# Kernel tuning notes

Measured on AMD Instinct MI355X. Metric: run time of the kernel, lower is better.

The kernel has to match this reference:

```python
import jax, jax.numpy as jnp
import numpy as np

D_MODEL = 1024
D_HEAD = 128
B, S = 4, 4096


def apply_rope(x, cos, sin):
    # x: [B,S,d_head], cos/sin: [S, d_head//2]
    half = x.shape[-1] // 2
    x1, x2 = x[..., :half], x[..., half:]
    cos = cos[None, :, :].astype(x.dtype)
    sin = sin[None, :, :].astype(x.dtype)
    return jnp.concatenate([x1 * cos - x2 * sin, x1 * sin + x2 * cos], axis=-1)


def setup_inputs() -> dict:
    key = jax.random.key(0)
    ks = jax.random.split(key, 10)
    x = jax.random.normal(ks[0], (B, S, D_MODEL), dtype=jnp.float32)
    # realistic RoPE tables
    half = D_HEAD // 2
    inv_freq = 1.0 / (10000.0 ** (np.arange(0, half, dtype=np.float32) / half))
    pos = np.arange(S, dtype=np.float32)
    ang = pos[:, None] * inv_freq[None, :]
    cos = jnp.asarray(np.cos(ang), dtype=jnp.float32)
    sin = jnp.asarray(np.sin(ang), dtype=jnp.float32)
    # True where key index > query index (masked positions)
    causal_mask = jnp.triu(jnp.ones((S, S), dtype=bool), k=1)
    scale_w = 1.0 / np.sqrt(D_MODEL)
    Wq1 = jax.random.normal(ks[1], (D_MODEL, D_HEAD), dtype=jnp.float32) * scale_w
    Wq2 = jax.random.normal(ks[2], (D_MODEL, D_HEAD), dtype=jnp.float32) * scale_w
    Wk1 = jax.random.normal(ks[3], (D_MODEL, D_HEAD), dtype=jnp.float32) * scale_w
    Wk2 = jax.random.normal(ks[4], (D_MODEL, D_HEAD), dtype=jnp.float32) * scale_w
    Wv = jax.random.normal(ks[5], (D_MODEL, D_HEAD), dtype=jnp.float32) * scale_w
    Wo = jax.random.normal(ks[6], (D_HEAD, D_MODEL), dtype=jnp.float32) * (1.0 / np.sqrt(D_HEAD))
    return {"x": x, "cos": cos, "sin": sin, "causal_mask": causal_mask,
            "Wq1": Wq1, "Wq2": Wq2, "Wk1": Wk1, "Wk2": Wk2, "Wv": Wv, "Wo": Wo}


def reference(x, cos, sin, causal_mask, Wq1, Wq2, Wk1, Wk2, Wv, Wo):
    q1 = apply_rope(jnp.einsum('bsD,Dd->bsd', x, Wq1), cos, sin)
    q2 = apply_rope(jnp.einsum('bsD,Dd->bsd', x, Wq2), cos, sin)
    k1 = apply_rope(jnp.einsum('bsD,Dd->bsd', x, Wk1), cos, sin)
    k2 = apply_rope(jnp.einsum('bsD,Dd->bsd', x, Wk2), cos, sin)
    v = jnp.einsum('bsD,Dd->bsd', x, Wv)
    scale = 1.0 / np.sqrt(D_HEAD)
    a1 = jnp.einsum('bsd,btd->bst', q1, k1) * scale
    a2 = jnp.einsum('bsd,btd->bst', q2, k2) * scale
    a = jnp.where(causal_mask[None, :, :], 0.0, a1 * a2)
    out = jnp.einsum('bst,btd->bsd', a, v)
    return jnp.einsum('bsd,dD->bsD', out, Wo)
```

## Files before the change

kernel.cpp:

```cpp
#include <hip/hip_runtime.h>
#include <stdint.h>
#include <stddef.h>

typedef _Float16 f16;
typedef __attribute__((ext_vector_type(8))) _Float16 f16x8;
typedef __attribute__((ext_vector_type(4))) _Float16 f16x4;
typedef __attribute__((ext_vector_type(16))) float f32x16;
typedef __attribute__((ext_vector_type(4))) float floatx4;

#define MFMA(a, b, c) __builtin_amdgcn_mfma_f32_32x32x16_f16((a), (b), (c), 0, 0, 0)

typedef const __attribute__((address_space(1))) void gvoid_t;
typedef __attribute__((address_space(3))) void svoid_t;

__device__ __forceinline__ void gload_lds16(const void* g, void* l) {
  __builtin_amdgcn_global_load_lds((gvoid_t*)g, (svoid_t*)l, 16, 0, 0);
}

__global__ __launch_bounds__(256) void k_wtrans(const float* __restrict__ W0,
                                                const float* __restrict__ W1,
                                                const float* __restrict__ W2,
                                                const float* __restrict__ W3,
                                                const float* __restrict__ W4,
                                                const float* __restrict__ Wo,
                                                f16* __restrict__ Wth,
                                                f16* __restrict__ Woth) {
  __shared__ float t[32][33];
  int bid = blockIdx.x;
  const float* W;
  f16* Wt;
  int K, N, k0, n0;
  if (bid < 640) {
    int w = bid >> 7, tt = bid & 127;
    W = (w == 0) ? W0 : (w == 1) ? W1 : (w == 2) ? W2 : (w == 3) ? W3 : W4;
    Wt = Wth + (size_t)w * 128 * 1024;
    K = 1024; N = 128;
    k0 = (tt & 31) * 32; n0 = (tt >> 5) * 32;
  } else {
    int tt = bid - 640;
    W = Wo; Wt = Woth;
    K = 128; N = 1024;
    k0 = (tt & 3) * 32; n0 = (tt >> 2) * 32;
  }
  int tx = threadIdx.x & 31, ty = threadIdx.x >> 5;
#pragma unroll
  for (int i = 0; i < 4; ++i)
    t[ty + 8 * i][tx] = W[(size_t)(k0 + ty + 8 * i) * N + n0 + tx];
  __syncthreads();
#pragma unroll
  for (int i = 0; i < 4; ++i)
    Wt[(size_t)(n0 + ty + 8 * i) * K + k0 + tx] = (f16)t[tx][ty + 8 * i];
}

__global__ __launch_bounds__(256, 2) void k_proj(const float* __restrict__ X,
                                                 const f16* __restrict__ Bt,
                                                 const float* __restrict__ cosp,
                                                 const float* __restrict__ sinp,
                                                 f16* __restrict__ q1h, f16* __restrict__ q2h,
                                                 f16* __restrict__ k1h, f16* __restrict__ k2h,
                                                 f16* __restrict__ vh) {
  __shared__ __align__(16) f16 As[128 * 64];
  __shared__ __align__(16) f16 Bs[128 * 64];
  int bid = blockIdx.x;
  int c8 = bid & 7, t = bid >> 3;
  int n0 = t % 5;
  int m0 = (c8 + 8 * (t / 5)) * 128;
  int tid = threadIdx.x;
  int wave = tid >> 6, lane = tid & 63;
  int wm = wave * 32;
  int rl = lane & 31, h = lane >> 5;
  int srow = lane >> 3, sslot = lane & 7;
  const f16* Bmat = Bt + (size_t)n0 * 128 * 1024;

  f32x16 acc[4];
#pragma unroll
  for (int nb = 0; nb < 4; ++nb)
#pragma unroll
    for (int r = 0; r < 16; ++r) acc[nb][r] = 0.f;

  for (int k0 = 0; k0 < 1024; k0 += 64) {
    __syncthreads();
#pragma unroll
    for (int c = 0; c < 4; ++c) {
      int chunk = c * 4 + wave;
      int r = chunk * 8 + srow;
      int cb = sslot ^ (r & 7);
      gload_lds16(Bmat + (size_t)r * 1024 + k0 + cb * 8, Bs + chunk * 512);
    }
#pragma unroll
    for (int c = 0; c < 4; ++c) {
      int chunk = c * 4 + wave;
      int r = chunk * 8 + srow;
      int cb = sslot ^ (r & 7);
      const float* src = X + (size_t)(m0 + r) * 1024 + k0 + cb * 8;
      floatx4 v0 = *(const floatx4*)src;
      floatx4 v1 = *(const floatx4*)(src + 4);
      f16x8 w;
#pragma unroll
      for (int e = 0; e < 4; ++e) { w[e] = (f16)v0[e]; w[e + 4] = (f16)v1[e]; }
      *(f16x8*)(As + chunk * 512 + srow * 64 + sslot * 8) = w;
    }
    __syncthreads();

#pragma unroll
    for (int kb = 0; kb < 4; ++kb) {
      int s = 2 * kb + h;
      int ra = wm + rl;
      f16x8 af = *(const f16x8*)(As + ra * 64 + (s ^ (ra & 7)) * 8);
      f16x8 bf[4];
#pragma unroll
      for (int nb = 0; nb < 4; ++nb) {
        int rb = nb * 32 + rl;
        bf[nb] = *(const f16x8*)(Bs + rb * 64 + (s ^ (rb & 7)) * 8);
      }
#pragma unroll
      for (int nb = 0; nb < 4; ++nb) acc[nb] = MFMA(af, bf[nb], acc[nb]);
    }
  }

  if (n0 == 4) {
#pragma unroll
    for (int r = 0; r < 16; ++r) {
      int irow = (r & 3) + 8 * (r >> 2) + 4 * h;
      int gr = m0 + wm + irow;
#pragma unroll
      for (int nb = 0; nb < 4; ++nb)
        vh[(size_t)gr * 128 + nb * 32 + rl] = (f16)acc[nb][r];
    }
  } else {
    f16* outp = (n0 == 0) ? q1h : (n0 == 1) ? q2h : (n0 == 2) ? k1h : k2h;
#pragma unroll
    for (int r = 0; r < 16; ++r) {
      int irow = (r & 3) + 8 * (r >> 2) + 4 * h;
      int gr = m0 + wm + irow;
      int s = gr & 4095;
#pragma unroll
      for (int nb = 0; nb < 2; ++nb) {
        int d = nb * 32 + rl;
        float c = cosp[s * 64 + d], sn = sinp[s * 64 + d];
        float a = acc[nb][r], bb = acc[nb + 2][r];
        outp[(size_t)gr * 128 + d]      = (f16)(a * c - bb * sn);
        outp[(size_t)gr * 128 + 64 + d] = (f16)(a * sn + bb * c);
      }
    }
  }
}

__global__ __launch_bounds__(256) void k_vtrans16(const f16* __restrict__ vh,
                                                  f16* __restrict__ vt) {
  __shared__ unsigned short t[32][33];
  int r0 = blockIdx.x * 32, d0 = blockIdx.y * 32;
  int tx = threadIdx.x & 31, ty = threadIdx.x >> 5;
#pragma unroll
  for (int i = 0; i < 4; ++i)
    t[ty + 8 * i][tx] = ((const unsigned short*)vh)[(size_t)(r0 + ty + 8 * i) * 128 + d0 + tx];
  __syncthreads();
  int b = r0 >> 12, s0 = r0 & 4095;
#pragma unroll
  for (int i = 0; i < 4; ++i)
    ((unsigned short*)vt)[((size_t)(b * 128 + d0 + ty + 8 * i)) * 4096 + s0 + tx] =
        t[tx][ty + 8 * i];
}

__global__ __launch_bounds__(256, 2) void k_s(const f16* __restrict__ q1h,
                                              const f16* __restrict__ q2h,
                                              const f16* __restrict__ k1h,
                                              const f16* __restrict__ k2h,
                                              f16* __restrict__ P) {
  __shared__ __align__(16) f16 A1[128 * 64];
  __shared__ __align__(16) f16 A2[128 * 64];
  __shared__ __align__(16) f16 B1[128 * 64];
  __shared__ __align__(16) f16 B2[128 * 64];
  int bid0 = blockIdx.x;
  int bid = (bid0 & 7) * 264 + (bid0 >> 3);
  int b = bid / 528, t = bid % 528;
  int i = (int)((sqrtf(8.f * t + 1.f) - 1.f) * 0.5f);
  if ((i + 1) * (i + 2) / 2 <= t) ++i;
  if (i * (i + 1) / 2 > t) --i;
  int j = t - i * (i + 1) / 2;

  int tid = threadIdx.x;
  int wave = tid >> 6, lane = tid & 63;
  int wm = (wave >> 1) * 64, wn = (wave & 1) * 64;
  int rl = lane & 31, h = lane >> 5;
  int srow = lane >> 3, sslot = lane & 7;
  size_t rowA = (size_t)b * 4096 + i * 128;
  size_t rowB = (size_t)b * 4096 + j * 128;

  f32x16 acc1[2][2], acc2[2][2];
#pragma unroll
  for (int mb = 0; mb < 2; ++mb)
#pragma unroll
    for (int nb = 0; nb < 2; ++nb)
#pragma unroll
      for (int r = 0; r < 16; ++r) { acc1[mb][nb][r] = 0.f; acc2[mb][nb][r] = 0.f; }

  for (int k0 = 0; k0 < 128; k0 += 64) {
    __syncthreads();
#pragma unroll
    for (int c = 0; c < 4; ++c) {
      int chunk = c * 4 + wave;
      int r = chunk * 8 + srow;
      int cb = sslot ^ (r & 7);
      gload_lds16(q1h + (rowA + r) * 128 + k0 + cb * 8, A1 + chunk * 512);
      gload_lds16(q2h + (rowA + r) * 128 + k0 + cb * 8, A2 + chunk * 512);
      gload_lds16(k1h + (rowB + r) * 128 + k0 + cb * 8, B1 + chunk * 512);
      gload_lds16(k2h + (rowB + r) * 128 + k0 + cb * 8, B2 + chunk * 512);
    }
    __syncthreads();

#pragma unroll
    for (int kb = 0; kb < 4; ++kb) {
      int s = 2 * kb + h;
      f16x8 a1f[2], a2f[2], b1f[2], b2f[2];
#pragma unroll
      for (int mb = 0; mb < 2; ++mb) {
        int r = wm + mb * 32 + rl;
        int off = r * 64 + (s ^ (r & 7)) * 8;
        a1f[mb] = *(const f16x8*)(A1 + off);
        a2f[mb] = *(const f16x8*)(A2 + off);
      }
#pragma unroll
      for (int nb = 0; nb < 2; ++nb) {
        int r = wn + nb * 32 + rl;
        int off = r * 64 + (s ^ (r & 7)) * 8;
        b1f[nb] = *(const f16x8*)(B1 + off);
        b2f[nb] = *(const f16x8*)(B2 + off);
      }
#pragma unroll
      for (int mb = 0; mb < 2; ++mb)
#pragma unroll
        for (int nb = 0; nb < 2; ++nb) {
          acc1[mb][nb] = MFMA(a1f[mb], b1f[nb], acc1[mb][nb]);
          acc2[mb][nb] = MFMA(a2f[mb], b2f[nb], acc2[mb][nb]);
        }
    }
  }

  f16* pt = P + ((size_t)b * 528 + t) * 16384;
  bool diag = (i == j);
#pragma unroll
  for (int mb = 0; mb < 2; ++mb)
#pragma unroll
    for (int nb = 0; nb < 2; ++nb)
#pragma unroll
      for (int r = 0; r < 16; ++r) {
        int row_l = wm + mb * 32 + (r & 3) + 8 * (r >> 2) + 4 * h;
        int col_l = wn + nb * 32 + rl;
        float p = acc1[mb][nb][r] * acc2[mb][nb][r] * (1.0f / 128.0f);
        if (diag && col_l > row_l) p = 0.f;
        pt[(size_t)row_l * 128 + col_l] = (f16)p;
      }
}

__global__ __launch_bounds__(256, 2) void k_pv(const f16* __restrict__ P,
                                               const f16* __restrict__ vt,
                                               f16* __restrict__ o0, f16* __restrict__ o1,
                                               f16* __restrict__ o2, f16* __restrict__ o3) {
  __shared__ __align__(16) f16 As[128 * 64];
  __shared__ __align__(16) f16 Bs[128 * 64];
  int bid = blockIdx.x;
  int b = bid / 80, c = bid % 80;
  int qt, s;
  if (c < 8)       { qt = c;                 s = 0; }
  else if (c < 24) { int t = c - 8;  qt = 8  + (t >> 1); s = t & 1; }
  else if (c < 48) { int t = c - 24; qt = 16 + t / 3;    s = t - 3 * (t / 3); }
  else             { int t = c - 48; qt = 24 + (t >> 2); s = t & 3; }
  int tq = qt * (qt + 1) / 2;
  const f16* Pb = P + (size_t)b * 528 * 16384;
  const f16* vb = vt + (size_t)b * 128 * 4096;
  int kbase = s * 1024;
  int kend = (qt + 1) * 128 < kbase + 1024 ? (qt + 1) * 128 : kbase + 1024;

  int tid = threadIdx.x;
  int wave = tid >> 6, lane = tid & 63;
  int wm = (wave >> 1) * 64, wn = (wave & 1) * 64;
  int rl = lane & 31, h = lane >> 5;
  int srow = lane >> 3, sslot = lane & 7;

  f32x16 acc[2][2];
#pragma unroll
  for (int mb = 0; mb < 2; ++mb)
#pragma unroll
    for (int nb = 0; nb < 2; ++nb)
#pragma unroll
      for (int r = 0; r < 16; ++r) acc[mb][nb][r] = 0.f;

  for (int k0 = kbase; k0 < kend; k0 += 64) {
    int jt = k0 >> 7, koff = k0 & 127;
    const f16* Pt = Pb + (size_t)(tq + jt) * 16384;
    __syncthreads();
#pragma unroll
    for (int c4 = 0; c4 < 4; ++c4) {
      int chunk = c4 * 4 + wave;
      int r = chunk * 8 + srow;
      int cb = sslot ^ (r & 7);
      gload_lds16(Pt + (size_t)r * 128 + koff + cb * 8, As + chunk * 512);
      gload_lds16(vb + (size_t)r * 4096 + k0 + cb * 8, Bs + chunk * 512);
    }
    __syncthreads();

#pragma unroll
    for (int kb = 0; kb < 4; ++kb) {
      int sidx = 2 * kb + h;
      f16x8 af[2], bf[2];
#pragma unroll
      for (int mb = 0; mb < 2; ++mb) {
        int r = wm + mb * 32 + rl;
        af[mb] = *(const f16x8*)(As + r * 64 + (sidx ^ (r & 7)) * 8);
      }
#pragma unroll
      for (int nb = 0; nb < 2; ++nb) {
        int r = wn + nb * 32 + rl;
        bf[nb] = *(const f16x8*)(Bs + r * 64 + (sidx ^ (r & 7)) * 8);
      }
#pragma unroll
      for (int mb = 0; mb < 2; ++mb)
#pragma unroll
        for (int nb = 0; nb < 2; ++nb)
          acc[mb][nb] = MFMA(af[mb], bf[nb], acc[mb][nb]);
    }
  }

  f16* op = (s == 0) ? o0 : (s == 1) ? o1 : (s == 2) ? o2 : o3;
#pragma unroll
  for (int mb = 0; mb < 2; ++mb)
#pragma unroll
    for (int nb = 0; nb < 2; ++nb)
#pragma unroll
      for (int r = 0; r < 16; ++r) {
        int gr = b * 4096 + qt * 128 + wm + mb * 32 + (r & 3) + 8 * (r >> 2) + 4 * h;
        op[(size_t)gr * 128 + wn + nb * 32 + rl] = (f16)acc[mb][nb][r];
      }
}

__global__ __launch_bounds__(256, 2) void k_gout(const f16* __restrict__ o0,
                                                 const f16* __restrict__ o1,
                                                 const f16* __restrict__ o2,
                                                 const f16* __restrict__ o3,
                                                 const f16* __restrict__ Bt,
                                                 float* __restrict__ C) {
  __shared__ __align__(16) f16 As[128 * 64];
  __shared__ __align__(16) f16 Bs[128 * 64];
  int tid = threadIdx.x;
  int wave = tid >> 6, lane = tid & 63;
  int m0 = blockIdx.y * 128, n0 = blockIdx.x * 128;
  int wm = (wave >> 1) * 64, wn = (wave & 1) * 64;
  int rl = lane & 31, h = lane >> 5;
  int srow = lane >> 3, sslot = lane & 7;
  int qt = (m0 >> 7) & 31;
  int ns = (qt >> 3) + 1;
  const f16* srcs[4] = {o0, o1, o2, o3};

  f32x16 acc[2][2];
#pragma unroll
  for (int mb = 0; mb < 2; ++mb)
#pragma unroll
    for (int nb = 0; nb < 2; ++nb)
#pragma unroll
      for (int r = 0; r < 16; ++r) acc[mb][nb][r] = 0.f;

  for (int k0 = 0; k0 < 128; k0 += 64) {
    __syncthreads();
#pragma unroll
    for (int c = 0; c < 4; ++c) {
      int chunk = c * 4 + wave;
      int r = chunk * 8 + srow;
      float sum[8];
#pragma unroll
      for (int e = 0; e < 8; ++e) sum[e] = 0.f;
#pragma unroll
      for (int p = 0; p < 4; ++p) {
        if (p < ns) {
          f16x8 v = *(const f16x8*)(srcs[p] + (size_t)(m0 + r) * 128 + k0 + sslot * 8);
#pragma unroll
          for (int e = 0; e < 8; ++e) sum[e] += (float)v[e];
        }
      }
      f16x8 w;
#pragma unroll
      for (int e = 0; e < 8; ++e) w[e] = (f16)sum[e];
      *(f16x8*)(As + r * 64 + (sslot ^ (r & 7)) * 8) = w;
      int cb = sslot ^ (r & 7);
      gload_lds16(Bt + (size_t)(n0 + r) * 128 + k0 + cb * 8, Bs + chunk * 512);
    }
    __syncthreads();

#pragma unroll
    for (int kb = 0; kb < 4; ++kb) {
      int s = 2 * kb + h;
      f16x8 af[2], bf[2];
#pragma unroll
      for (int mb = 0; mb < 2; ++mb) {
        int r = wm + mb * 32 + rl;
        af[mb] = *(const f16x8*)(As + r * 64 + (s ^ (r & 7)) * 8);
      }
#pragma unroll
      for (int nb = 0; nb < 2; ++nb) {
        int r = wn + nb * 32 + rl;
        bf[nb] = *(const f16x8*)(Bs + r * 64 + (s ^ (r & 7)) * 8);
      }
#pragma unroll
      for (int mb = 0; mb < 2; ++mb)
#pragma unroll
        for (int nb = 0; nb < 2; ++nb)
          acc[mb][nb] = MFMA(af[mb], bf[nb], acc[mb][nb]);
    }
  }

#pragma unroll
  for (int mb = 0; mb < 2; ++mb)
#pragma unroll
    for (int nb = 0; nb < 2; ++nb)
#pragma unroll
      for (int r = 0; r < 16; ++r) {
        int i = m0 + wm + mb * 32 + (r & 3) + 8 * (r >> 2) + 4 * h;
        int j = n0 + wn + nb * 32 + rl;
        C[(size_t)i * 1024 + j] = acc[mb][nb][r];
      }
}

extern "C" void kernel_launch(void* const* d_in, const int* in_sizes, int n_in,
                              void* d_out, int out_size, void* d_ws, size_t ws_size,
                              hipStream_t stream) {
  (void)in_sizes; (void)n_in; (void)out_size; (void)ws_size;
  const float* x  = (const float*)d_in[0];
  const float* cp = (const float*)d_in[1];
  const float* sp = (const float*)d_in[2];
  const float* W[5] = {(const float*)d_in[4], (const float*)d_in[5], (const float*)d_in[6],
                       (const float*)d_in[7], (const float*)d_in[8]};
  const float* Wo = (const float*)d_in[9];
  float* out = (float*)d_out;
  char* ws = (char*)d_ws;

  const size_t OFF_H    = 16777216;
  const size_t OFF_WTH  = OFF_H + 6 * 4194304;
  const size_t OFF_WOTH = OFF_WTH + 1310720;
  const size_t OFF_P    = OFF_WOTH + 262144;
  f16*   o0   = (f16*)(ws + 0);
  f16*   o1   = (f16*)(ws + 4194304);
  f16*   o2   = (f16*)(ws + 8388608);
  f16*   o3   = (f16*)(ws + 12582912);
  f16*   q1h  = (f16*)(ws + OFF_H + 0 * 4194304);
  f16*   q2h  = (f16*)(ws + OFF_H + 1 * 4194304);
  f16*   k1h  = (f16*)(ws + OFF_H + 2 * 4194304);
  f16*   k2h  = (f16*)(ws + OFF_H + 3 * 4194304);
  f16*   vh   = (f16*)(ws + OFF_H + 4 * 4194304);
  f16*   vt   = (f16*)(ws + OFF_H + 5 * 4194304);
  f16*   Wth  = (f16*)(ws + OFF_WTH);
  f16*   Woth = (f16*)(ws + OFF_WOTH);
  f16*   P    = (f16*)(ws + OFF_P);

  k_wtrans<<<768, 256, 0, stream>>>(W[0], W[1], W[2], W[3], W[4], Wo, Wth, Woth);
  k_proj<<<640, 256, 0, stream>>>(x, Wth, cp, sp, q1h, q2h, k1h, k2h, vh);
  k_vtrans16<<<dim3(512, 4), 256, 0, stream>>>(vh, vt);
  k_s<<<2112, 256, 0, stream>>>(q1h, q2h, k1h, k2h, P);
  k_pv<<<320, 256, 0, stream>>>(P, vt, o0, o1, o2, o3);
  k_gout<<<dim3(8, 128), 256, 0, stream>>>(o0, o1, o2, o3, Woth, out);
}
```

Before: 143.4 us.

## Double-buffer projection GEMM and split PV reduction into finer K-chunks

The projection kernel now double-buffers its LDS tiles and prefetches the next X/W tile into registers and LDS while MFMAs run on the current one, so there is one barrier per K step instead of two. The PV kernel splits the key range into 512-wide chunks instead of 1024, raising the block count from 320 to 576 for better load balance on the triangular work. Partial outputs are addressed from a single base with up to eight slices, and the output kernel sums up to eight partials. This costs more LDS in k_proj, which may reduce occupancy, plus extra partial-sum traffic in k_gout.

```diff
diff --git a/kernel.cpp b/kernel.cpp
--- a/kernel.cpp
+++ b/kernel.cpp
@@ -59,17 +59,18 @@
                                                  f16* __restrict__ q1h, f16* __restrict__ q2h,
                                                  f16* __restrict__ k1h, f16* __restrict__ k2h,
                                                  f16* __restrict__ vh) {
-  __shared__ __align__(16) f16 As[128 * 64];
-  __shared__ __align__(16) f16 Bs[128 * 64];
+  __shared__ __align__(16) f16 As[2][128 * 64];
+  __shared__ __align__(16) f16 Bs[2][128 * 64];
   int bid = blockIdx.x;
-  int c8 = bid & 7, t = bid >> 3;
-  int n0 = t % 5;
-  int m0 = (c8 + 8 * (t / 5)) * 128;
+  int c8 = bid & 7, tt = bid >> 3;
+  int n0 = tt % 5;
+  int m0 = (c8 + 8 * (tt / 5)) * 128;
   int tid = threadIdx.x;
   int wave = tid >> 6, lane = tid & 63;
   int wm = wave * 32;
   int rl = lane & 31, h = lane >> 5;
   int srow = lane >> 3, sslot = lane & 7;
+  int wslot = sslot ^ srow;
   const f16* Bmat = Bt + (size_t)n0 * 128 * 1024;
 
   f32x16 acc[4];
@@ -78,45 +79,52 @@
 #pragma unroll
     for (int r = 0; r < 16; ++r) acc[nb][r] = 0.f;
 
-  for (int k0 = 0; k0 < 1024; k0 += 64) {
-    __syncthreads();
-#pragma unroll
-    for (int c = 0; c < 4; ++c) {
-      int chunk = c * 4 + wave;
-      int r = chunk * 8 + srow;
-      int cb = sslot ^ (r & 7);
-      gload_lds16(Bmat + (size_t)r * 1024 + k0 + cb * 8, Bs + chunk * 512);
-    }
-#pragma unroll
-    for (int c = 0; c < 4; ++c) {
-      int chunk = c * 4 + wave;
-      int r = chunk * 8 + srow;
-      int cb = sslot ^ (r & 7);
-      const float* src = X + (size_t)(m0 + r) * 1024 + k0 + cb * 8;
-      floatx4 v0 = *(const floatx4*)src;
-      floatx4 v1 = *(const floatx4*)(src + 4);
-      f16x8 w;
-#pragma unroll
-      for (int e = 0; e < 4; ++e) { w[e] = (f16)v0[e]; w[e + 4] = (f16)v1[e]; }
-      *(f16x8*)(As + chunk * 512 + srow * 64 + sslot * 8) = w;
-    }
-    __syncthreads();
-
+  floatx4 pa[4][2];
+
+#define LOADA(k0_) do { _Pragma("unroll") for (int c = 0; c < 4; ++c) { \
+    int chunk = c * 4 + wave; int r = chunk * 8 + srow; \
+    const float* src = X + (size_t)(m0 + r) * 1024 + (k0_) + sslot * 8; \
+    pa[c][0] = *(const floatx4*)src; pa[c][1] = *(const floatx4*)(src + 4); } } while (0)
+#define WRITEA(bufi) do { _Pragma("unroll") for (int c = 0; c < 4; ++c) { \
+    int chunk = c * 4 + wave; \
+    f16x8 w; _Pragma("unroll") for (int e = 0; e < 4; ++e) { \
+      w[e] = (f16)pa[c][0][e]; w[e + 4] = (f16)pa[c][1][e]; } \
+    *(f16x8*)(As[bufi] + chunk * 512 + srow * 64 + wslot * 8) = w; } } while (0)
+#define LOADB(k0_, bufi) do { _Pragma("unroll") for (int c = 0; c < 4; ++c) { \
+    int chunk = c * 4 + wave; int r = chunk * 8 + srow; int cb = sslot ^ (r & 7); \
+    gload_lds16(Bmat + (size_t)r * 1024 + (k0_) + cb * 8, Bs[bufi] + chunk * 512); } } while (0)
+
+  LOADB(0, 0);
+  LOADA(0);
+  WRITEA(0);
+  __syncthreads();
+
+  for (int t = 0; t < 16; ++t) {
+    int cur = t & 1;
+    if (t < 15) {
+      LOADB(64 * (t + 1), cur ^ 1);
+      LOADA(64 * (t + 1));
+    }
 #pragma unroll
     for (int kb = 0; kb < 4; ++kb) {
       int s = 2 * kb + h;
       int ra = wm + rl;
-      f16x8 af = *(const f16x8*)(As + ra * 64 + (s ^ (ra & 7)) * 8);
+      f16x8 af = *(const f16x8*)(As[cur] + ra * 64 + (s ^ (ra & 7)) * 8);
       f16x8 bf[4];
 #pragma unroll
       for (int nb = 0; nb < 4; ++nb) {
-        int rb = nb * 32 + rl;
-        bf[nb] = *(const f16x8*)(Bs + rb * 64 + (s ^ (rb & 7)) * 8);
+        int rb2 = nb * 32 + rl;
+        bf[nb] = *(const f16x8*)(Bs[cur] + rb2 * 64 + (s ^ (rb2 & 7)) * 8);
       }
 #pragma unroll
       for (int nb = 0; nb < 4; ++nb) acc[nb] = MFMA(af, bf[nb], acc[nb]);
     }
-  }
+    if (t < 15) WRITEA(cur ^ 1);
+    __syncthreads();
+  }
+#undef LOADA
+#undef WRITEA
+#undef LOADB
 
   if (n0 == 4) {
 #pragma unroll
@@ -255,22 +263,22 @@
 
 __global__ __launch_bounds__(256, 2) void k_pv(const f16* __restrict__ P,
                                                const f16* __restrict__ vt,
-                                               f16* __restrict__ o0, f16* __restrict__ o1,
-                                               f16* __restrict__ o2, f16* __restrict__ o3) {
+                                               f16* __restrict__ obase) {
   __shared__ __align__(16) f16 As[128 * 64];
   __shared__ __align__(16) f16 Bs[128 * 64];
   int bid = blockIdx.x;
-  int b = bid / 80, c = bid % 80;
-  int qt, s;
-  if (c < 8)       { qt = c;                 s = 0; }
-  else if (c < 24) { int t = c - 8;  qt = 8  + (t >> 1); s = t & 1; }
-  else if (c < 48) { int t = c - 24; qt = 16 + t / 3;    s = t - 3 * (t / 3); }
-  else             { int t = c - 48; qt = 24 + (t >> 2); s = t & 3; }
+  int b = bid / 144, c = bid % 144;
+  int g = (int)((sqrtf(2.f * c + 1.f) - 1.f) * 0.5f);
+  while (2 * (g + 1) * (g + 2) <= c) ++g;
+  while (2 * g * (g + 1) > c) --g;
+  int off = c - 2 * g * (g + 1);
+  int qt = g * 4 + off / (g + 1);
+  int s = off - (off / (g + 1)) * (g + 1);
   int tq = qt * (qt + 1) / 2;
   const f16* Pb = P + (size_t)b * 528 * 16384;
   const f16* vb = vt + (size_t)b * 128 * 4096;
-  int kbase = s * 1024;
-  int kend = (qt + 1) * 128 < kbase + 1024 ? (qt + 1) * 128 : kbase + 1024;
+  int kbase = s * 512;
+  int kend = (qt + 1) * 128 < kbase + 512 ? (qt + 1) * 128 : kbase + 512;
 
   int tid = threadIdx.x;
   int wave = tid >> 6, lane = tid & 63;
@@ -322,7 +330,7 @@
     }
   }
 
-  f16* op = (s == 0) ? o0 : (s == 1) ? o1 : (s == 2) ? o2 : o3;
+  f16* op = obase + (size_t)s * 2097152;
 #pragma unroll
   for (int mb = 0; mb < 2; ++mb)
 #pragma unroll
@@ -334,10 +342,7 @@
       }
 }
 
-__global__ __launch_bounds__(256, 2) void k_gout(const f16* __restrict__ o0,
-                                                 const f16* __restrict__ o1,
-                                                 const f16* __restrict__ o2,
-                                                 const f16* __restrict__ o3,
+__global__ __launch_bounds__(256, 2) void k_gout(const f16* __restrict__ obase,
                                                  const f16* __restrict__ Bt,
                                                  float* __restrict__ C) {
   __shared__ __align__(16) f16 As[128 * 64];
@@ -349,8 +354,7 @@
   int rl = lane & 31, h = lane >> 5;
   int srow = lane >> 3, sslot = lane & 7;
   int qt = (m0 >> 7) & 31;
-  int ns = (qt >> 3) + 1;
-  const f16* srcs[4] = {o0, o1, o2, o3};
+  int ns = (qt >> 2) + 1;
 
   f32x16 acc[2][2];
 #pragma unroll
@@ -370,9 +374,10 @@
 #pragma unroll
       for (int e = 0; e < 8; ++e) sum[e] = 0.f;
 #pragma unroll
-      for (int p = 0; p < 4; ++p) {
+      for (int p = 0; p < 8; ++p) {
         if (p < ns) {
-          f16x8 v = *(const f16x8*)(srcs[p] + (size_t)(m0 + r) * 128 + k0 + sslot * 8);
+          f16x8 v = *(const f16x8*)(obase + (size_t)p * 2097152 +
+                                    (size_t)(m0 + r) * 128 + k0 + sslot * 8);
 #pragma unroll
           for (int e = 0; e < 8; ++e) sum[e] += (float)v[e];
         }
@@ -433,14 +438,11 @@
   float* out = (float*)d_out;
   char* ws = (char*)d_ws;
 
-  const size_t OFF_H    = 16777216;
+  const size_t OFF_H    = 33554432;
   const size_t OFF_WTH  = OFF_H + 6 * 4194304;
   const size_t OFF_WOTH = OFF_WTH + 1310720;
   const size_t OFF_P    = OFF_WOTH + 262144;
-  f16*   o0   = (f16*)(ws + 0);
-  f16*   o1   = (f16*)(ws + 4194304);
-  f16*   o2   = (f16*)(ws + 8388608);
-  f16*   o3   = (f16*)(ws + 12582912);
+  f16*   obase = (f16*)(ws + 0);
   f16*   q1h  = (f16*)(ws + OFF_H + 0 * 4194304);
   f16*   q2h  = (f16*)(ws + OFF_H + 1 * 4194304);
   f16*   k1h  = (f16*)(ws + OFF_H + 2 * 4194304);
@@ -455,6 +457,6 @@
   k_proj<<<640, 256, 0, stream>>>(x, Wth, cp, sp, q1h, q2h, k1h, k2h, vh);
   k_vtrans16<<<dim3(512, 4), 256, 0, stream>>>(vh, vt);
   k_s<<<2112, 256, 0, stream>>>(q1h, q2h, k1h, k2h, P);
-  k_pv<<<320, 256, 0, stream>>>(P, vt, o0, o1, o2, o3);
-  k_gout<<<dim3(8, 128), 256, 0, stream>>>(o0, o1, o2, o3, Woth, out);
-}
+  k_pv<<<576, 256, 0, stream>>>(P, vt, obase);
+  k_gout<<<dim3(8, 128), 256, 0, stream>>>(obase, Woth, out);
+}
```

Result: slower. 164.7 us (+14.8%).
